# Optimization experiments

Hardware: AMD Instinct MI355X
Metric: run time of the kernel (lower is better)

The kernel has to match this reference:

```python
import jax, jax.numpy as jnp
import numpy as np

EPS = 0.05
ITERS = 100
TOL = 1e-4
LN_EPS = 1e-5


def _ln(x, s, b):
    m = x.mean(-1, keepdims=True)
    v = ((x - m) ** 2).mean(-1, keepdims=True)
    return (x - m) / jnp.sqrt(v + LN_EPS) * s + b


def _sinkhorn(M):
    # M: [N, HW] raw logits (fp32). Entropic OT with uniform marginals.
    n, hw = M.shape
    log_K = M / EPS
    log_mu = jnp.log(1.0 / n + 1e-8)
    log_nu = jnp.log(1.0 / hw + 1e-8)

    def cond(st):
        i, lu, lv, diff = st
        return (i < ITERS) & (diff >= TOL)

    def body(st):
        i, lu, lv, _ = st
        new_lu = log_mu - jax.scipy.special.logsumexp(log_K + lv[None, :], axis=1)
        new_lv = log_nu - jax.scipy.special.logsumexp(log_K + new_lu[:, None], axis=0)
        return (i + 1, new_lu, new_lv, jnp.max(jnp.abs(new_lu - lu)))

    st0 = (jnp.int32(0), jnp.zeros((n,), jnp.float32), jnp.zeros((hw,), jnp.float32), jnp.float32(jnp.inf))
    _, lu, lv, _ = jax.lax.while_loop(cond, body, st0)
    log_T = lu[:, None] + log_K + lv[None, :]
    return jnp.clip(jnp.exp(log_T), 0.0, 1.0)


def setup_inputs() -> dict:
    key = jax.random.key(0)
    ks = jax.random.split(key, 12)
    B, C, H, W, N = 16, 256, 64, 64, 5
    E = 2 * C
    w = lambda k, sh: (jax.random.normal(k, sh, jnp.float32) * 0.02)
    return {
        'Fd': jax.random.normal(ks[0], (B, C, H, W), jnp.float32),
        'prompts': w(ks[1], (N, C)),
        'sa_q_w': w(ks[2], (C, C)), 'sa_q_b': jnp.zeros((C,), jnp.float32),
        'sa_k_w': w(ks[3], (C, C)), 'sa_k_b': jnp.zeros((C,), jnp.float32),
        'sa_v_w': w(ks[4], (C, C)), 'sa_v_b': jnp.zeros((C,), jnp.float32),
        'sa_ln_s': jnp.ones((C,), jnp.float32), 'sa_ln_b': jnp.zeros((C,), jnp.float32),
        'wq_w': w(ks[5], (C, C)), 'wq_b': jnp.zeros((C,), jnp.float32),
        'wk_w': w(ks[6], (C, C)), 'wk_b': jnp.zeros((C,), jnp.float32),
        'wv_w': w(ks[7], (C, C)), 'wv_b': jnp.zeros((C,), jnp.float32),
        'ca_ln_s': jnp.ones((C,), jnp.float32), 'ca_ln_b': jnp.zeros((C,), jnp.float32),
        'ffn_w1': w(ks[8], (C, E)), 'ffn_b1': jnp.zeros((E,), jnp.float32),
        'ffn_w2': w(ks[9], (E, C)), 'ffn_b2': jnp.zeros((C,), jnp.float32),
        'ffn_ln_s': jnp.ones((C,), jnp.float32), 'ffn_ln_b': jnp.zeros((C,), jnp.float32),
    }


def reference(Fd, prompts, sa_q_w, sa_q_b, sa_k_w, sa_k_b, sa_v_w, sa_v_b,
              sa_ln_s, sa_ln_b, wq_w, wq_b, wk_w, wk_b, wv_w, wv_b,
              ca_ln_s, ca_ln_b, ffn_w1, ffn_b1, ffn_w2, ffn_b2, ffn_ln_s, ffn_ln_b):
    B, C, H, W = Fd.shape
    scale = C ** -0.5
    Fd_flat = Fd.transpose(0, 2, 3, 1).reshape(B, H * W, C)  # [B, HW, C]
    P = jnp.broadcast_to(prompts[None], (B,) + prompts.shape)  # [B, N, C]

    # self-attention over prompts
    Q = P @ sa_q_w + sa_q_b
    K = P @ sa_k_w + sa_k_b
    V = P @ sa_v_w + sa_v_b
    attn = jax.nn.softmax(jnp.einsum('bnc,bmc->bnm', Q, K) * scale, axis=-1)
    P = _ln(P + jnp.einsum('bnm,bmc->bnc', attn, V), sa_ln_s, sa_ln_b)

    # cross-attention prompts -> pixels
    Qc = P @ wq_w + wq_b                 # [B, N, C]
    Kc = Fd_flat @ wk_w + wk_b           # [B, HW, C]
    Vc = Fd_flat @ wv_w + wv_b           # [B, HW, C]
    logits = jnp.einsum('bnc,bmc->bnm', Qc, Kc) * scale  # [B, N, HW]
    M = jax.nn.softmax(logits, axis=-1)
    P = _ln(P + jnp.einsum('bnm,bmc->bnc', M, Vc), ca_ln_s, ca_ln_b)

    # OT regularization: Sinkhorn on detached logits, BCE(M, T*)
    T = jax.vmap(_sinkhorn)(jax.lax.stop_gradient(logits))
    Mc = jnp.clip(M, 1e-6, 1.0 - 1e-6)
    bce = -(T * jnp.log(Mc) + (1.0 - T) * jnp.log(1.0 - Mc))
    L_ot = bce.mean(axis=(1, 2)).mean()

    # FFN + residual + LN
    h = jax.nn.gelu(P @ ffn_w1 + ffn_b1, approximate=False) @ ffn_w2 + ffn_b2
    P_hat = _ln(P + h, ffn_ln_s, ffn_ln_b)
    return (P_hat, L_ot)
```

## Files before the change

kernel.cpp:

```cpp
#include <hip/hip_runtime.h>
#include <hip/hip_fp16.h>
#include <math.h>

#define LOG2E 1.44269504088896340f
#define LN2   0.69314718055994531f

__device__ __forceinline__ float warpReduceSum(float v){
#pragma unroll
    for (int off = 32; off > 0; off >>= 1) v += __shfl_down(v, off);
    return v;
}
__device__ __forceinline__ float warpReduceMax(float v){
#pragma unroll
    for (int off = 32; off > 0; off >>= 1) v = fmaxf(v, __shfl_down(v, off));
    return v;
}

__device__ float blockSum256(float v, float* s4){
    v = warpReduceSum(v);
    int w = threadIdx.x >> 6;
    __syncthreads();
    if ((threadIdx.x & 63) == 0) s4[w] = v;
    __syncthreads();
    return s4[0] + s4[1] + s4[2] + s4[3];
}
__device__ float blockSum512(float v, float* s8){
    v = warpReduceSum(v);
    int w = threadIdx.x >> 6;
    __syncthreads();
    if ((threadIdx.x & 63) == 0) s8[w] = v;
    __syncthreads();
    float s = 0.f;
#pragma unroll
    for (int i = 0; i < 8; i++) s += s8[i];
    return s;
}

__global__ __launch_bounds__(256) void k_qkv(
    const float* __restrict__ prompts,
    const float* __restrict__ qw, const float* __restrict__ qb,
    const float* __restrict__ kw, const float* __restrict__ kb,
    const float* __restrict__ vw, const float* __restrict__ vb,
    float* __restrict__ QKV)
{
    __shared__ float Pl[1280];
    __shared__ float parts[4][5][64];
    int t = threadIdx.x;
    int mat = blockIdx.x >> 2, chunk = blockIdx.x & 3;
    for (int i = t; i < 1280; i += 256) Pl[i] = prompts[i];
    const float* W  = (mat == 0) ? qw : (mat == 1) ? kw : vw;
    const float* Bv = (mat == 0) ? qb : (mat == 1) ? kb : vb;
    int cl = t & 63, p = t >> 6;
    int col = chunk*64 + cl;
    __syncthreads();
    float acc[5] = {0,0,0,0,0};
    const float* wp = W + (size_t)(p*64)*256 + col;
#pragma unroll 8
    for (int c = 0; c < 64; c++){
        float wv = wp[(size_t)c*256];
#pragma unroll
        for (int n = 0; n < 5; n++) acc[n] += Pl[n*256 + p*64 + c] * wv;
    }
#pragma unroll
    for (int n = 0; n < 5; n++) parts[p][n][cl] = acc[n];
    __syncthreads();
    for (int i = t; i < 320; i += 256){
        int n = i >> 6, c2 = i & 63;
        float s = parts[0][n][c2] + parts[1][n][c2] + parts[2][n][c2] + parts[3][n][c2]
                + Bv[chunk*64 + c2];
        QKV[mat*1280 + n*256 + chunk*64 + c2] = s;
    }
}

__global__ __launch_bounds__(256) void k_attn(
    const float* __restrict__ QKV, const float* __restrict__ prompts,
    const float* __restrict__ lns, const float* __restrict__ lnb,
    float* __restrict__ P1g)
{
    __shared__ float Pl[1280], Ql[1280], Kl[1280], Vl[1280], Sl[25], s4[4];
    int t = threadIdx.x;
    for (int i = t; i < 1280; i += 256){
        Pl[i] = prompts[i];
        Ql[i] = QKV[i];
        Kl[i] = QKV[1280 + i];
        Vl[i] = QKV[2560 + i];
    }
    __syncthreads();
    if (t < 25){
        int n = t / 5, m = t % 5;
        float s = 0.f;
        for (int c = 0; c < 256; c++) s += Ql[n*256 + c] * Kl[m*256 + c];
        Sl[t] = s * 0.0625f;
    }
    __syncthreads();
    if (t < 5){
        float mx = -1e30f;
        for (int m = 0; m < 5; m++) mx = fmaxf(mx, Sl[t*5 + m]);
        float e[5], sm = 0.f;
        for (int m = 0; m < 5; m++){ e[m] = expf(Sl[t*5 + m] - mx); sm += e[m]; }
        for (int m = 0; m < 5; m++) Sl[t*5 + m] = e[m] / sm;
    }
    __syncthreads();
    float x[5];
#pragma unroll
    for (int n = 0; n < 5; n++){
        float s = 0.f;
        for (int m = 0; m < 5; m++) s += Sl[n*5 + m] * Vl[m*256 + t];
        x[n] = Pl[n*256 + t] + s;
    }
#pragma unroll
    for (int n = 0; n < 5; n++){
        float sum  = blockSum256(x[n], s4);
        float mean = sum * (1.0f/256.0f);
        float d    = x[n] - mean;
        float sq   = blockSum256(d*d, s4);
        float rstd = rsqrtf(sq * (1.0f/256.0f) + 1e-5f);
        P1g[n*256 + t] = d * rstd * lns[t] + lnb[t];
    }
}

__global__ __launch_bounds__(256) void k_qc(
    const float* __restrict__ P1, const float* __restrict__ wqw,
    const float* __restrict__ wqb, float* __restrict__ Qcg)
{
    __shared__ float Pr[256];
    int n = blockIdx.x, t = threadIdx.x;
    Pr[t] = P1[n*256 + t];
    __syncthreads();
    float acc = wqb[t];
    const float* wp = wqw + t;
#pragma unroll 16
    for (int d = 0; d < 256; d++) acc += Pr[d] * wp[(size_t)d*256];
    Qcg[n*256 + t] = acc;
}

__global__ __launch_bounds__(256) void k_qk2(
    const float* __restrict__ Qc, const float* __restrict__ wkw,
    const float* __restrict__ wkb,
    float* __restrict__ qkg, float* __restrict__ qkbg)
{
    __shared__ float Qr[256], s4[4];
    int n = blockIdx.y, t = threadIdx.x;
    int w = t >> 6, lane = t & 63;
    Qr[t] = Qc[n*256 + t];
    __syncthreads();
#pragma unroll
    for (int i = 0; i < 4; i++){
        int c = blockIdx.x*16 + w*4 + i;
        const float* kp = wkw + (size_t)c*256;
        float acc = Qr[lane]       * kp[lane]
                  + Qr[lane + 64]  * kp[lane + 64]
                  + Qr[lane + 128] * kp[lane + 128]
                  + Qr[lane + 192] * kp[lane + 192];
#pragma unroll
        for (int off = 1; off < 64; off <<= 1) acc += __shfl_xor(acc, off);
        if (lane == 0) qkg[n*256 + c] = acc;
    }
    if (blockIdx.x == 0){
        float pu = blockSum256(Qr[t] * wkb[t], s4);
        if (t == 0) qkbg[n] = pu;
    }
}

__global__ __launch_bounds__(1024) void k_logits(
    const float* __restrict__ Fd, const float* __restrict__ qkg,
    const float* __restrict__ qkbg, float* __restrict__ logits)
{
    __shared__ float qk[1280];
    __shared__ float qb5[5];
    __shared__ float parts[4][5][256];
    int t = threadIdx.x;
    for (int i = t; i < 1280; i += 1024) qk[i] = qkg[i];
    if (t < 5) qb5[t] = qkbg[t];
    __syncthreads();
    int b = blockIdx.y;
    int p = t >> 8, ml = t & 255;
    int m = blockIdx.x * 256 + ml;
    const float* fp = Fd + ((size_t)(b*256 + p*64)) * 4096 + m;
    float a0 = 0.f, a1 = 0.f, a2 = 0.f, a3 = 0.f, a4 = 0.f;
#pragma unroll 16
    for (int c = 0; c < 64; c++){
        float f = fp[(size_t)c * 4096];
        a0 += qk[          p*64 + c] * f;
        a1 += qk[256  +    p*64 + c] * f;
        a2 += qk[512  +    p*64 + c] * f;
        a3 += qk[768  +    p*64 + c] * f;
        a4 += qk[1024 +    p*64 + c] * f;
    }
    parts[p][0][ml] = a0; parts[p][1][ml] = a1; parts[p][2][ml] = a2;
    parts[p][3][ml] = a3; parts[p][4][ml] = a4;
    __syncthreads();
    for (int i = t; i < 1280; i += 1024){
        int n = i >> 8, mm = i & 255;
        float s = parts[0][n][mm] + parts[1][n][mm] + parts[2][n][mm] + parts[3][n][mm]
                + qb5[n];
        logits[((size_t)(b*5) + n)*4096 + blockIdx.x*256 + mm] = s * 0.0625f;
    }
}

__global__ __launch_bounds__(1024) void k_A(
    const float* __restrict__ Fd, const float* __restrict__ logits,
    float* __restrict__ A)
{
    __shared__ __align__(16) __half Ml[5*4096];
    __shared__ float red[80];
    int b = blockIdx.y, cc = blockIdx.x, t = threadIdx.x;
    int w = t >> 6, lane = t & 63;
    const float* Lb = logits + (size_t)(b*5) * 4096;
    float ll[5][4];
#pragma unroll
    for (int n = 0; n < 5; n++)
#pragma unroll
        for (int k = 0; k < 4; k++)
            ll[n][k] = Lb[n*4096 + t + k*1024];
#pragma unroll
    for (int n = 0; n < 5; n++){
        float tm = fmaxf(fmaxf(ll[n][0], ll[n][1]), fmaxf(ll[n][2], ll[n][3]));
        tm = warpReduceMax(tm);
        if (lane == 0) red[w*5 + n] = tm;
    }
    __syncthreads();
    float mx[5];
#pragma unroll
    for (int n = 0; n < 5; n++){
        float gm = -1e30f;
        for (int i = 0; i < 16; i++) gm = fmaxf(gm, red[i*5 + n]);
        mx[n] = gm;
    }
    __syncthreads();
    float e[5][4];
#pragma unroll
    for (int n = 0; n < 5; n++){
        float ps = 0.f;
#pragma unroll
        for (int k = 0; k < 4; k++){ e[n][k] = expf(ll[n][k] - mx[n]); ps += e[n][k]; }
        ps = warpReduceSum(ps);
        if (lane == 0) red[w*5 + n] = ps;
    }
    __syncthreads();
#pragma unroll
    for (int n = 0; n < 5; n++){
        float z = 0.f;
        for (int i = 0; i < 16; i++) z += red[i*5 + n];
        float inv = 1.0f / z;
#pragma unroll
        for (int k = 0; k < 4; k++)
            Ml[n*4096 + t + k*1024] = __float2half(e[n][k] * inv);
    }
    __syncthreads();
    int c = cc*16 + w;
    const float* fp = Fd + ((size_t)(b*256 + c)) * 4096;
    float4 a4[5];
#pragma unroll
    for (int n = 0; n < 5; n++) a4[n] = make_float4(0.f, 0.f, 0.f, 0.f);
#pragma unroll 4
    for (int it = 0; it < 16; it++){
        int m4 = it*256 + (lane << 2);
        float4 f = *(const float4*)(fp + m4);
#pragma unroll
        for (int n = 0; n < 5; n++){
            const __half2* mp = (const __half2*)(Ml + n*4096 + m4);
            float2 m0 = __half22float2(mp[0]);
            float2 m1 = __half22float2(mp[1]);
            a4[n].x += m0.x * f.x; a4[n].y += m0.y * f.y;
            a4[n].z += m1.x * f.z; a4[n].w += m1.y * f.w;
        }
    }
#pragma unroll
    for (int n = 0; n < 5; n++){
        float s = a4[n].x + a4[n].y + a4[n].z + a4[n].w;
        s = warpReduceSum(s);
        if (lane == 0) A[(size_t)(b*5 + n)*256 + c] = s;
    }
}

__global__ __launch_bounds__(1024) void k_sinkhorn(
    const float* __restrict__ logits, float* __restrict__ out_l)
{
    __shared__ float redm[2][16][5], reds[16][5];
    __shared__ float redb[16];
    int b = blockIdx.x, t = threadIdx.x;
    int w = t >> 6, lane = t & 63;
    const float* Lb = logits + (size_t)b * 5 * 4096;
    float lk2[5][4], ek[5][4];
#pragma unroll
    for (int n = 0; n < 5; n++)
#pragma unroll
        for (int k = 0; k < 4; k++){
            float lv = (Lb[n*4096 + t + k*1024] / 0.05f) * LOG2E;
            lk2[n][k] = lv;
            ek[n][k] = exp2f(lv);
        }
    const float mu_lin  = 0.2f + 1e-8f;
    const float nu_lin  = 1.0f/4096.0f + 1e-8f;
    const float log2mu  = log2f(mu_lin);
    const float log2nu  = log2f(nu_lin);
    const float TOL2    = 1e-4f * LOG2E;

    float vv[4]  = {1.f, 1.f, 1.f, 1.f};
    float lu2[5] = {0,0,0,0,0};
    float lv2[4] = {0,0,0,0};
    float en[5];
    float diff = 1e30f;
    int par = 0;

    for (int it = 0; it < 100; ++it){
        if (diff < TOL2) break;
        float gs[5];
#pragma unroll
        for (int n = 0; n < 5; n++)
            gs[n] = ek[n][0]*vv[0] + ek[n][1]*vv[1] + ek[n][2]*vv[2] + ek[n][3]*vv[3];
#pragma unroll
        for (int off = 1; off < 64; off <<= 1){
#pragma unroll
            for (int n = 0; n < 5; n++) gs[n] += __shfl_xor(gs[n], off);
        }
        if (lane == 0){
#pragma unroll
            for (int n = 0; n < 5; n++) redm[par][w][n] = gs[n];
        }
        __syncthreads();
        float nd = 0.f;
#pragma unroll
        for (int n = 0; n < 5; n++){
            float s = 0.f;
            for (int i = 0; i < 16; i++) s += redm[par][i][n];
            float nl = log2mu - log2f(s);
            nd = fmaxf(nd, fabsf(nl - lu2[n]));
            lu2[n] = nl;
            en[n] = mu_lin / s;
        }
        diff = nd;
#pragma unroll
        for (int k = 0; k < 4; k++){
            float cs = ek[0][k]*en[0] + ek[1][k]*en[1] + ek[2][k]*en[2]
                     + ek[3][k]*en[3] + ek[4][k]*en[4];
            vv[k]  = nu_lin / cs;
            lv2[k] = log2nu - log2f(cs);
        }
        par ^= 1;
    }
    __syncthreads();

    float tm[5];
#pragma unroll
    for (int n = 0; n < 5; n++){
        float l0 = lk2[n][0]*0.05f, l1 = lk2[n][1]*0.05f;
        float l2 = lk2[n][2]*0.05f, l3 = lk2[n][3]*0.05f;
        tm[n] = fmaxf(fmaxf(l0, l1), fmaxf(l2, l3));
    }
#pragma unroll
    for (int off = 1; off < 64; off <<= 1){
#pragma unroll
        for (int n = 0; n < 5; n++) tm[n] = fmaxf(tm[n], __shfl_xor(tm[n], off));
    }
    if (lane == 0){
#pragma unroll
        for (int n = 0; n < 5; n++) redm[0][w][n] = tm[n];
    }
    __syncthreads();
    float mx5[5];
#pragma unroll
    for (int n = 0; n < 5; n++){
        float gm = -1e30f;
        for (int i = 0; i < 16; i++) gm = fmaxf(gm, redm[0][i][n]);
        mx5[n] = gm;
    }
    float pz[5];
#pragma unroll
    for (int n = 0; n < 5; n++){
        pz[n] = exp2f(lk2[n][0]*0.05f - mx5[n]) + exp2f(lk2[n][1]*0.05f - mx5[n])
              + exp2f(lk2[n][2]*0.05f - mx5[n]) + exp2f(lk2[n][3]*0.05f - mx5[n]);
    }
#pragma unroll
    for (int off = 1; off < 64; off <<= 1){
#pragma unroll
        for (int n = 0; n < 5; n++) pz[n] += __shfl_xor(pz[n], off);
    }
    if (lane == 0){
#pragma unroll
        for (int n = 0; n < 5; n++) reds[w][n] = pz[n];
    }
    __syncthreads();
    float iz5[5];
#pragma unroll
    for (int n = 0; n < 5; n++){
        float z = 0.f;
        for (int i = 0; i < 16; i++) z += reds[i][n];
        iz5[n] = 1.0f / z;
    }
    float acc = 0.f;
#pragma unroll
    for (int n = 0; n < 5; n++){
#pragma unroll
        for (int k = 0; k < 4; k++){
            float Mv = exp2f(lk2[n][k]*0.05f - mx5[n]) * iz5[n];
            float Mc = fminf(fmaxf(Mv, 1e-6f), 1.0f - 1e-6f);
            float lT2 = lu2[n] + lk2[n][k] + lv2[k];
            float T  = fminf(exp2f(lT2), 1.0f);
            acc -= (T * log2f(Mc) + (1.0f - T) * log2f(1.0f - Mc)) * LN2;
        }
    }
    acc = warpReduceSum(acc);
    if (lane == 0) redb[w] = acc;
    __syncthreads();
    if (t == 0){
        float s = 0.f;
        for (int i = 0; i < 16; i++) s += redb[i];
        atomicAdd(out_l, s * (1.0f / (16.0f * 5.0f * 4096.0f)));
    }
}

__global__ __launch_bounds__(512) void k_epilogue(
    const float* __restrict__ A, const float* __restrict__ P1,
    const float* __restrict__ wvw, const float* __restrict__ wvb,
    const float* __restrict__ clns, const float* __restrict__ clnb,
    const float* __restrict__ w1, const float* __restrict__ b1,
    const float* __restrict__ w2, const float* __restrict__ b2,
    const float* __restrict__ flns, const float* __restrict__ flnb,
    float* __restrict__ out)
{
    __shared__ float Ar[256], P1r[256], P2[256], hl[512], parts[2][256], s8[8];
    int bn = blockIdx.x;
    int n = bn % 5;
    int t = threadIdx.x;
    if (t < 256){ Ar[t] = A[(size_t)bn*256 + t]; P1r[t] = P1[n*256 + t]; }
    __syncthreads();
    int c = t & 255, p = t >> 8;
    {
        float acc = 0.f;
        const float* wp = wvw + (size_t)(p*128)*256 + c;
#pragma unroll 16
        for (int k = 0; k < 128; k++) acc += Ar[p*128 + k] * wp[(size_t)k*256];
        parts[p][c] = acc;
    }
    __syncthreads();
    float x = 0.f;
    if (t < 256) x = P1r[t] + parts[0][t] + parts[1][t] + wvb[t];
    float sum  = blockSum512((t < 256) ? x : 0.f, s8);
    float mean = sum * (1.0f/256.0f);
    float d    = x - mean;
    float sq   = blockSum512((t < 256) ? d*d : 0.f, s8);
    float rstd = rsqrtf(sq * (1.0f/256.0f) + 1e-5f);
    float p2v = 0.f;
    if (t < 256){
        p2v = d * rstd * clns[t] + clnb[t];
        P2[t] = p2v;
    }
    __syncthreads();
    {
        float a = b1[t];
        const float* wp = w1 + t;
#pragma unroll 16
        for (int k = 0; k < 256; k++) a += P2[k] * wp[(size_t)k*512];
        hl[t] = 0.5f * a * (1.0f + erff(a * 0.70710678118654752f));
    }
    __syncthreads();
    {
        float acc = 0.f;
        const float* wp = w2 + (size_t)(p*256)*256 + c;
#pragma unroll 16
        for (int k = 0; k < 256; k++) acc += hl[p*256 + k] * wp[(size_t)k*256];
        parts[p][c] = acc;
    }
    __syncthreads();
    float x2 = 0.f;
    if (t < 256) x2 = P2[t] + parts[0][t] + parts[1][t] + b2[t];
    float sum2  = blockSum512((t < 256) ? x2 : 0.f, s8);
    float mean2 = sum2 * (1.0f/256.0f);
    float d2    = x2 - mean2;
    float sq2   = blockSum512((t < 256) ? d2*d2 : 0.f, s8);
    float rstd2 = rsqrtf(sq2 * (1.0f/256.0f) + 1e-5f);
    if (t < 256) out[(size_t)bn*256 + t] = d2 * rstd2 * flns[t] + flnb[t];
}

extern "C" void kernel_launch(void* const* d_in, const int* in_sizes, int n_in,
                              void* d_out, int out_size, void* d_ws, size_t ws_size,
                              hipStream_t stream)
{
    const float* Fd      = (const float*)d_in[0];
    const float* prompts = (const float*)d_in[1];
    const float* sa_q_w  = (const float*)d_in[2];
    const float* sa_q_b  = (const float*)d_in[3];
    const float* sa_k_w  = (const float*)d_in[4];
    const float* sa_k_b  = (const float*)d_in[5];
    const float* sa_v_w  = (const float*)d_in[6];
    const float* sa_v_b  = (const float*)d_in[7];
    const float* sa_ln_s = (const float*)d_in[8];
    const float* sa_ln_b = (const float*)d_in[9];
    const float* wq_w    = (const float*)d_in[10];
    const float* wq_b    = (const float*)d_in[11];
    const float* wk_w    = (const float*)d_in[12];
    const float* wk_b    = (const float*)d_in[13];
    const float* wv_w    = (const float*)d_in[14];
    const float* wv_b    = (const float*)d_in[15];
    const float* ca_ln_s = (const float*)d_in[16];
    const float* ca_ln_b = (const float*)d_in[17];
    const float* ffn_w1  = (const float*)d_in[18];
    const float* ffn_b1  = (const float*)d_in[19];
    const float* ffn_w2  = (const float*)d_in[20];
    const float* ffn_b2  = (const float*)d_in[21];
    const float* ffn_ln_s= (const float*)d_in[22];
    const float* ffn_ln_b= (const float*)d_in[23];

    float* out = (float*)d_out;
    float* ws  = (float*)d_ws;

    float* P1     = ws;
    float* qkb    = ws + 1536;
    float* QKV    = ws + 2048;
    float* Qc     = ws + 6144;
    float* qkg    = ws + 8192;
    float* logits = ws + 73728;
    float* Amat   = ws + 401408;

    hipMemsetAsync(out + 20480, 0, sizeof(float), stream);

    k_qkv<<<12, 256, 0, stream>>>(prompts, sa_q_w, sa_q_b, sa_k_w, sa_k_b,
                                  sa_v_w, sa_v_b, QKV);
    k_attn<<<1, 256, 0, stream>>>(QKV, prompts, sa_ln_s, sa_ln_b, P1);
    k_qc<<<5, 256, 0, stream>>>(P1, wq_w, wq_b, Qc);
    k_qk2<<<dim3(16, 5), 256, 0, stream>>>(Qc, wk_w, wk_b, qkg, qkb);
    k_logits<<<dim3(16, 16), 1024, 0, stream>>>(Fd, qkg, qkb, logits);
    k_A<<<dim3(16, 16), 1024, 0, stream>>>(Fd, logits, Amat);
    k_sinkhorn<<<16, 1024, 0, stream>>>(logits, out + 20480);
    k_epilogue<<<80, 512, 0, stream>>>(Amat, P1, wv_w, wv_b, ca_ln_s, ca_ln_b,
                                       ffn_w1, ffn_b1, ffn_w2, ffn_b2,
                                       ffn_ln_s, ffn_ln_b, out);
}
```

Before: 256.4 us.

## Fuse attention with Qc projection, drop log-domain Sinkhorn state and memset

Merges the prompt self-attention kernel with the Qc projection into one 5-block launch, each block recomputing the attention and layer norm redundantly. In the Sinkhorn loop the per-iteration log2 tracking of u and v is removed and convergence is tested on the linear scaling factors with a relative threshold. The transport plan is then built from products of the linear factors, and the cross-warp reductions use transposed shared arrays read as float4. The atomicAdd and memset for the loss are replaced by per-batch partials summed in the epilogue kernel, saving one launch and a memset at the cost of slightly different convergence and precision behaviour.

```diff
diff --git a/kernel.cpp b/kernel.cpp
--- a/kernel.cpp
+++ b/kernel.cpp
@@ -72,10 +72,11 @@
     }
 }
 
-__global__ __launch_bounds__(256) void k_attn(
+__global__ __launch_bounds__(256) void k_attn_qc(
     const float* __restrict__ QKV, const float* __restrict__ prompts,
     const float* __restrict__ lns, const float* __restrict__ lnb,
-    float* __restrict__ P1g)
+    const float* __restrict__ wqw, const float* __restrict__ wqb,
+    float* __restrict__ P1g, float* __restrict__ Qcg)
 {
     __shared__ float Pl[1280], Ql[1280], Kl[1280], Vl[1280], Sl[25], s4[4];
     int t = threadIdx.x;
@@ -115,22 +116,16 @@
         float d    = x[n] - mean;
         float sq   = blockSum256(d*d, s4);
         float rstd = rsqrtf(sq * (1.0f/256.0f) + 1e-5f);
-        P1g[n*256 + t] = d * rstd * lns[t] + lnb[t];
-    }
-}
-
-__global__ __launch_bounds__(256) void k_qc(
-    const float* __restrict__ P1, const float* __restrict__ wqw,
-    const float* __restrict__ wqb, float* __restrict__ Qcg)
-{
-    __shared__ float Pr[256];
-    int n = blockIdx.x, t = threadIdx.x;
-    Pr[t] = P1[n*256 + t];
-    __syncthreads();
+        float y = d * rstd * lns[t] + lnb[t];
+        Pl[n*256 + t] = y;
+        if (blockIdx.x == 0) P1g[n*256 + t] = y;
+    }
+    __syncthreads();
+    int n = blockIdx.x;
     float acc = wqb[t];
     const float* wp = wqw + t;
 #pragma unroll 16
-    for (int d = 0; d < 256; d++) acc += Pr[d] * wp[(size_t)d*256];
+    for (int d = 0; d < 256; d++) acc += Pl[n*256 + d] * wp[(size_t)d*256];
     Qcg[n*256 + t] = acc;
 }
 
@@ -275,9 +270,10 @@
 }
 
 __global__ __launch_bounds__(1024) void k_sinkhorn(
-    const float* __restrict__ logits, float* __restrict__ out_l)
-{
-    __shared__ float redm[2][16][5], reds[16][5];
+    const float* __restrict__ logits, float* __restrict__ partial)
+{
+    __shared__ __align__(16) float redm[2][5][16];
+    __shared__ __align__(16) float reds[5][16];
     __shared__ float redb[16];
     int b = blockIdx.x, t = threadIdx.x;
     int w = t >> 6, lane = t & 63;
@@ -293,19 +289,16 @@
         }
     const float mu_lin  = 0.2f + 1e-8f;
     const float nu_lin  = 1.0f/4096.0f + 1e-8f;
-    const float log2mu  = log2f(mu_lin);
-    const float log2nu  = log2f(nu_lin);
-    const float TOL2    = 1e-4f * LOG2E;
+    const float thr     = 1.00005e-4f;
 
     float vv[4]  = {1.f, 1.f, 1.f, 1.f};
-    float lu2[5] = {0,0,0,0,0};
-    float lv2[4] = {0,0,0,0};
+    float en_prev[5] = {1.f, 1.f, 1.f, 1.f, 1.f};
     float en[5];
     float diff = 1e30f;
     int par = 0;
 
     for (int it = 0; it < 100; ++it){
-        if (diff < TOL2) break;
+        if (diff < 0.f) break;
         float gs[5];
 #pragma unroll
         for (int n = 0; n < 5; n++)
@@ -317,26 +310,27 @@
         }
         if (lane == 0){
 #pragma unroll
-            for (int n = 0; n < 5; n++) redm[par][w][n] = gs[n];
+            for (int n = 0; n < 5; n++) redm[par][n][w] = gs[n];
         }
         __syncthreads();
-        float nd = 0.f;
+        float slack = -1.f;
 #pragma unroll
         for (int n = 0; n < 5; n++){
-            float s = 0.f;
-            for (int i = 0; i < 16; i++) s += redm[par][i][n];
-            float nl = log2mu - log2f(s);
-            nd = fmaxf(nd, fabsf(nl - lu2[n]));
-            lu2[n] = nl;
-            en[n] = mu_lin / s;
-        }
-        diff = nd;
+            const float4* rp = (const float4*)redm[par][n];
+            float4 A4 = rp[0], B4 = rp[1], C4 = rp[2], D4 = rp[3];
+            float s = (((A4.x+A4.y)+(A4.z+A4.w)) + ((B4.x+B4.y)+(B4.z+B4.w)))
+                    + (((C4.x+C4.y)+(C4.z+C4.w)) + ((D4.x+D4.y)+(D4.z+D4.w)));
+            float e = mu_lin / s;
+            slack = fmaxf(slack, fabsf(e - en_prev[n]) - thr * en_prev[n]);
+            en_prev[n] = e;
+            en[n] = e;
+        }
+        diff = slack;
 #pragma unroll
         for (int k = 0; k < 4; k++){
             float cs = ek[0][k]*en[0] + ek[1][k]*en[1] + ek[2][k]*en[2]
                      + ek[3][k]*en[3] + ek[4][k]*en[4];
-            vv[k]  = nu_lin / cs;
-            lv2[k] = log2nu - log2f(cs);
+            vv[k] = nu_lin / cs;
         }
         par ^= 1;
     }
@@ -356,14 +350,18 @@
     }
     if (lane == 0){
 #pragma unroll
-        for (int n = 0; n < 5; n++) redm[0][w][n] = tm[n];
+        for (int n = 0; n < 5; n++) redm[0][n][w] = tm[n];
     }
     __syncthreads();
     float mx5[5];
 #pragma unroll
     for (int n = 0; n < 5; n++){
-        float gm = -1e30f;
-        for (int i = 0; i < 16; i++) gm = fmaxf(gm, redm[0][i][n]);
+        const float4* rp = (const float4*)redm[0][n];
+        float4 A4 = rp[0], B4 = rp[1], C4 = rp[2], D4 = rp[3];
+        float gm = fmaxf(fmaxf(fmaxf(A4.x,A4.y), fmaxf(A4.z,A4.w)),
+                         fmaxf(fmaxf(B4.x,B4.y), fmaxf(B4.z,B4.w)));
+        gm = fmaxf(gm, fmaxf(fmaxf(fmaxf(C4.x,C4.y), fmaxf(C4.z,C4.w)),
+                             fmaxf(fmaxf(D4.x,D4.y), fmaxf(D4.z,D4.w))));
         mx5[n] = gm;
     }
     float pz[5];
@@ -379,14 +377,16 @@
     }
     if (lane == 0){
 #pragma unroll
-        for (int n = 0; n < 5; n++) reds[w][n] = pz[n];
+        for (int n = 0; n < 5; n++) reds[n][w] = pz[n];
     }
     __syncthreads();
     float iz5[5];
 #pragma unroll
     for (int n = 0; n < 5; n++){
-        float z = 0.f;
-        for (int i = 0; i < 16; i++) z += reds[i][n];
+        const float4* rp = (const float4*)reds[n];
+        float4 A4 = rp[0], B4 = rp[1], C4 = rp[2], D4 = rp[3];
+        float z = (((A4.x+A4.y)+(A4.z+A4.w)) + ((B4.x+B4.y)+(B4.z+B4.w)))
+                + (((C4.x+C4.y)+(C4.z+C4.w)) + ((D4.x+D4.y)+(D4.z+D4.w)));
         iz5[n] = 1.0f / z;
     }
     float acc = 0.f;
@@ -396,8 +396,7 @@
         for (int k = 0; k < 4; k++){
             float Mv = exp2f(lk2[n][k]*0.05f - mx5[n]) * iz5[n];
             float Mc = fminf(fmaxf(Mv, 1e-6f), 1.0f - 1e-6f);
-            float lT2 = lu2[n] + lk2[n][k] + lv2[k];
-            float T  = fminf(exp2f(lT2), 1.0f);
+            float T  = fminf(en[n] * ek[n][k] * vv[k], 1.0f);
             acc -= (T * log2f(Mc) + (1.0f - T) * log2f(1.0f - Mc)) * LN2;
         }
     }
@@ -407,7 +406,7 @@
     if (t == 0){
         float s = 0.f;
         for (int i = 0; i < 16; i++) s += redb[i];
-        atomicAdd(out_l, s * (1.0f / (16.0f * 5.0f * 4096.0f)));
+        partial[b] = s;
     }
 }
 
@@ -418,12 +417,18 @@
     const float* __restrict__ w1, const float* __restrict__ b1,
     const float* __restrict__ w2, const float* __restrict__ b2,
     const float* __restrict__ flns, const float* __restrict__ flnb,
+    const float* __restrict__ sink_part,
     float* __restrict__ out)
 {
     __shared__ float Ar[256], P1r[256], P2[256], hl[512], parts[2][256], s8[8];
     int bn = blockIdx.x;
     int n = bn % 5;
     int t = threadIdx.x;
+    if (bn == 0 && t == 0){
+        float s = 0.f;
+        for (int i = 0; i < 16; i++) s += sink_part[i];
+        out[20480] = s * (1.0f / (16.0f * 5.0f * 4096.0f));
+    }
     if (t < 256){ Ar[t] = A[(size_t)bn*256 + t]; P1r[t] = P1[n*256 + t]; }
     __syncthreads();
     int c = t & 255, p = t >> 8;
@@ -511,20 +516,19 @@
     float* QKV    = ws + 2048;
     float* Qc     = ws + 6144;
     float* qkg    = ws + 8192;
+    float* spart  = ws + 9472;
     float* logits = ws + 73728;
     float* Amat   = ws + 401408;
 
-    hipMemsetAsync(out + 20480, 0, sizeof(float), stream);
-
     k_qkv<<<12, 256, 0, stream>>>(prompts, sa_q_w, sa_q_b, sa_k_w, sa_k_b,
                                   sa_v_w, sa_v_b, QKV);
-    k_attn<<<1, 256, 0, stream>>>(QKV, prompts, sa_ln_s, sa_ln_b, P1);
-    k_qc<<<5, 256, 0, stream>>>(P1, wq_w, wq_b, Qc);
+    k_attn_qc<<<5, 256, 0, stream>>>(QKV, prompts, sa_ln_s, sa_ln_b,
+                                     wq_w, wq_b, P1, Qc);
     k_qk2<<<dim3(16, 5), 256, 0, stream>>>(Qc, wk_w, wk_b, qkg, qkb);
     k_logits<<<dim3(16, 16), 1024, 0, stream>>>(Fd, qkg, qkb, logits);
     k_A<<<dim3(16, 16), 1024, 0, stream>>>(Fd, logits, Amat);
-    k_sinkhorn<<<16, 1024, 0, stream>>>(logits, out + 20480);
+    k_sinkhorn<<<16, 1024, 0, stream>>>(logits, spart);
     k_epilogue<<<80, 512, 0, stream>>>(Amat, P1, wv_w, wv_b, ca_ln_s, ca_ln_b,
                                        ffn_w1, ffn_b1, ffn_w2, ffn_b2,
-                                       ffn_ln_s, ffn_ln_b, out);
-}
+                                       ffn_ln_s, ffn_ln_b, spart, out);
+}
```

New measurement: 247.1 us. -3.6%, faster.
